# Optimization experiments

Hardware: AMD Instinct MI355X
Metric: run time of the kernel (lower is better)

Reference implementation:

```python
import jax, jax.numpy as jnp
import numpy as np

N_NODES = 50000
N_EDGES = 600000
H_DIM = 128
N_RELS = 8
N_BASES = 4


def setup_inputs() -> dict:
    key = jax.random.key(0)
    ks = jax.random.split(key, 12)
    feats = jax.random.normal(ks[0], (N_NODES, H_DIM), dtype=jnp.float32)
    src = jax.random.randint(ks[1], (N_EDGES,), 0, N_NODES, dtype=jnp.int64)
    dst = jax.random.randint(ks[2], (N_EDGES,), 0, N_NODES, dtype=jnp.int64)
    etype = jax.random.randint(ks[3], (N_EDGES,), 0, N_RELS, dtype=jnp.int64)
    norm = jax.random.uniform(ks[4], (N_EDGES, 1), dtype=jnp.float32)
    s = 1.0 / np.sqrt(H_DIM)
    # layer 0 params (basis decomposition: W_r = sum_b comp[r,b] * basis[b])
    basis0 = jax.random.normal(ks[5], (N_BASES, H_DIM, H_DIM), dtype=jnp.float32) * s
    comp0 = jax.random.normal(ks[6], (N_RELS, N_BASES), dtype=jnp.float32)
    bias0 = jnp.zeros((H_DIM,), dtype=jnp.float32)
    # layer 1 params
    basis1 = jax.random.normal(ks[7], (N_BASES, H_DIM, H_DIM), dtype=jnp.float32) * s
    comp1 = jax.random.normal(ks[8], (N_RELS, N_BASES), dtype=jnp.float32)
    bias1 = jnp.zeros((H_DIM,), dtype=jnp.float32)
    return {"feats": feats, "src": src, "dst": dst, "etype": etype, "norm": norm,
            "basis0": basis0, "comp0": comp0, "bias0": bias0,
            "basis1": basis1, "comp1": comp1, "bias1": bias1}


def _rel_graph_conv(h, src, dst, etype, norm, basis, comp, bias):
    # basis-decomposed relation weights: [R, d_in, d_out]
    W = jnp.einsum('rb,bdo->rdo', comp, basis)
    # transform all nodes under every relation: [R, N, d_out]
    Hr = jnp.einsum('nd,rdo->rno', h, W)
    # gather per-edge message by (relation, source node), apply edge norm
    msg = Hr[etype, src] * norm  # [E, d_out]
    # scatter-sum into destination nodes
    agg = jax.ops.segment_sum(msg, dst, num_segments=h.shape[0])
    return jax.nn.relu(agg + bias)


def reference(feats, src, dst, etype, norm, basis0, comp0, bias0, basis1, comp1, bias1):
    h = _rel_graph_conv(feats, src, dst, etype, norm, basis0, comp0, bias0)
    h = _rel_graph_conv(h, src, dst, etype, norm, basis1, comp1, bias1)
    return h
```

## Files before the change

### kernel.cpp

```cpp
#include <hip/hip_runtime.h>

#define H    128
#define NB   4
#define DT   32

typedef __attribute__((ext_vector_type(8))) short short8;
typedef __attribute__((ext_vector_type(4))) float f32x4;

static __device__ __forceinline__ unsigned short f2bf(float f) {
    unsigned u = __float_as_uint(f);
    unsigned r = (u + 0x7fffu + ((u >> 16) & 1u)) >> 16;
    return (unsigned short)r;
}
static __device__ __forceinline__ float bf_lo(unsigned v) {
    return __uint_as_float((v & 0xffffu) << 16);
}
static __device__ __forceinline__ float bf_hi(unsigned v) {
    return __uint_as_float(v & 0xffff0000u);
}
static __device__ __forceinline__ float bfe(short s) {
    return __uint_as_float(((unsigned)(unsigned short)s) << 16);
}

__global__ __launch_bounds__(256) void zero_i(int* __restrict__ p, int n) {
    int i = blockIdx.x * 256 + threadIdx.x;
    if (i < n) p[i] = 0;
}

__global__ __launch_bounds__(256) void hist_rank(const int* __restrict__ dst,
                                                 int* __restrict__ counts,
                                                 int* __restrict__ rank, int E) {
    int e = blockIdx.x * 256 + threadIdx.x;
    if (e < E) rank[e] = atomicAdd(&counts[dst[e]], 1);
}

__global__ __launch_bounds__(1024) void scan_blocks(const int* __restrict__ counts,
                                                    int* __restrict__ partial,
                                                    int* __restrict__ blocksums, int n) {
    __shared__ int buf[1024];
    int tid = threadIdx.x;
    int i = blockIdx.x * 1024 + tid;
    buf[tid] = (i < n) ? counts[i] : 0;
    __syncthreads();
#pragma unroll
    for (int off = 1; off < 1024; off <<= 1) {
        int t = (tid >= off) ? buf[tid - off] : 0;
        __syncthreads();
        buf[tid] += t;
        __syncthreads();
    }
    if (i < n) partial[i] = buf[tid];
    if (tid == 1023) blocksums[blockIdx.x] = buf[1023];
}

__global__ __launch_bounds__(64) void scan_carry(int* __restrict__ blocksums, int nb) {
    int tid = threadIdx.x;
    int v = (tid < nb) ? blocksums[tid] : 0;
#pragma unroll
    for (int off = 1; off < 64; off <<= 1) {
        int t = __shfl_up(v, off);
        if (tid >= off) v += t;
    }
    if (tid < nb) blocksums[tid] = v;
}

__global__ __launch_bounds__(256) void scan_add(const int* __restrict__ partial,
                                                const int* __restrict__ blocksums,
                                                int* __restrict__ offs, int n) {
    int i = blockIdx.x * 256 + threadIdx.x;
    if (i >= n) return;
    int b = i >> 10;
    int carry = (b > 0) ? blocksums[b - 1] : 0;
    offs[i + 1] = partial[i] + carry;
    if (i == 0) offs[0] = 0;
}

__global__ __launch_bounds__(256) void scatter_edges(
        const int* __restrict__ src, const int* __restrict__ dst,
        const int* __restrict__ etype, const float* __restrict__ norm,
        const float* __restrict__ comp0, const float* __restrict__ comp1,
        const int* __restrict__ offs, const int* __restrict__ rank,
        uint4* __restrict__ er0, uint4* __restrict__ er1, int E) {
    int e = blockIdx.x * 256 + threadIdx.x;
    if (e >= E) return;
    int pos = offs[dst[e]] + rank[e];
    float w = norm[e];
    int et = etype[e];
    float4 c0 = *(const float4*)(comp0 + et * NB);
    float4 c1 = *(const float4*)(comp1 + et * NB);
    uint4 r0, r1;
    r0.x = (unsigned)src[e];
    r0.y = (unsigned)f2bf(w * c0.x) | ((unsigned)f2bf(w * c0.y) << 16);
    r0.z = (unsigned)f2bf(w * c0.z) | ((unsigned)f2bf(w * c0.w) << 16);
    r0.w = 0;
    r1.x = (unsigned)src[e];
    r1.y = (unsigned)f2bf(w * c1.x) | ((unsigned)f2bf(w * c1.y) << 16);
    r1.z = (unsigned)f2bf(w * c1.z) | ((unsigned)f2bf(w * c1.w) << 16);
    r1.w = 0;
    er0[pos] = r0;
    er1[pos] = r1;
}

__global__ __launch_bounds__(256) void convert_bf16(const float* __restrict__ in,
                                                    unsigned short* __restrict__ out, int n4) {
    int i = blockIdx.x * 256 + threadIdx.x;
    if (i >= n4) return;
    float4 v = ((const float4*)in)[i];
    ushort4 o;
    o.x = f2bf(v.x); o.y = f2bf(v.y); o.z = f2bf(v.z); o.w = f2bf(v.w);
    ((ushort4*)out)[i] = o;
}

__global__ __launch_bounds__(128) void make_wb(
        const float* __restrict__ basis0, const float* __restrict__ basis1,
        unsigned short* __restrict__ Wb) {
    int b = blockIdx.x;
    int d = blockIdx.y;
    int l = blockIdx.z;
    int o = threadIdx.x;
    const float* basis = l ? basis1 : basis0;
    float s = basis[((size_t)b * H + d) * H + o];
    Wb[((size_t)l * H + o) * (NB * H) + b * H + d] = f2bf(s);
}

#define EDGE_ACC(REC, HV) {                                             \
    float wa = bf_lo(REC.y), wb = bf_hi(REC.y);                         \
    float wc = bf_lo(REC.z), wd = bf_hi(REC.z);                         \
    _Pragma("unroll")                                                   \
    for (int c = 0; c < 8; ++c) {                                       \
        float f = bfe(HV[c]);                                           \
        a0[c] = fmaf(wa, f, a0[c]); a1[c] = fmaf(wb, f, a1[c]);         \
        a2[c] = fmaf(wc, f, a2[c]); a3[c] = fmaf(wd, f, a3[c]);         \
    } }

__global__ __launch_bounds__(512) void fused_layer(
        const unsigned short* __restrict__ hin,
        const int* __restrict__ offs,
        const uint4* __restrict__ er,
        const unsigned short* __restrict__ Wb,
        const float* __restrict__ bias,
        void* __restrict__ outp, int M, int write_bf16) {
    __shared__ char lds[DT * 1024];
    const int tid  = threadIdx.x;
    const int nl   = tid >> 4;
    const int ch   = tid & 15;
    const int v0   = blockIdx.x * DT;
    const int v    = v0 + nl;

    float a0[8], a1[8], a2[8], a3[8];
#pragma unroll
    for (int c = 0; c < 8; ++c) { a0[c] = 0.f; a1[c] = 0.f; a2[c] = 0.f; a3[c] = 0.f; }

    if (v < M) {
        const int beg = offs[v], end = offs[v + 1];
        int e = beg;
        for (; e + 2 <= end; e += 2) {
            uint4 r0 = er[e];
            uint4 r1 = er[e + 1];
            short8 h0 = *(const short8*)(hin + (size_t)r0.x * H + ch * 8);
            short8 h1 = *(const short8*)(hin + (size_t)r1.x * H + ch * 8);
            EDGE_ACC(r0, h0)
            EDGE_ACC(r1, h1)
        }
        if (e < end) {
            uint4 r0 = er[e];
            short8 h0 = *(const short8*)(hin + (size_t)r0.x * H + ch * 8);
            EDGE_ACC(r0, h0)
        }
    }

    {
        char* row = lds + nl * 1024;
        const int swz = (nl & 7) << 4;
        uint4 pk;
#define PACK(A) pk.x = (unsigned)f2bf(A[0]) | ((unsigned)f2bf(A[1]) << 16); \
                pk.y = (unsigned)f2bf(A[2]) | ((unsigned)f2bf(A[3]) << 16); \
                pk.z = (unsigned)f2bf(A[4]) | ((unsigned)f2bf(A[5]) << 16); \
                pk.w = (unsigned)f2bf(A[6]) | ((unsigned)f2bf(A[7]) << 16);
        PACK(a0) *(uint4*)(row + ((0 * 256 + ch * 16) ^ swz)) = pk;
        PACK(a1) *(uint4*)(row + ((1 * 256 + ch * 16) ^ swz)) = pk;
        PACK(a2) *(uint4*)(row + ((2 * 256 + ch * 16) ^ swz)) = pk;
        PACK(a3) *(uint4*)(row + ((3 * 256 + ch * 16) ^ swz)) = pk;
#undef PACK
    }
    __syncthreads();

    const int wid  = tid >> 6;
    const int lane = tid & 63;
    const int n0 = wid * 16;
    const int lr = lane & 15;
    const int lg = lane >> 4;
    const char* bbase = (const char*)Wb + (size_t)(n0 + lr) * (NB * H) * 2;
    const int swz = (lr & 7) << 4;

    f32x4 acc0 = (f32x4){0.f, 0.f, 0.f, 0.f};
    f32x4 acc1 = (f32x4){0.f, 0.f, 0.f, 0.f};
#pragma unroll
    for (int ks = 0; ks < 16; ++ks) {
        const int kb = ks * 64 + lg * 16;
        short8 b  = *(const short8*)(bbase + kb);
        short8 av0 = *(const short8*)(lds + (lr)      * 1024 + (kb ^ swz));
        short8 av1 = *(const short8*)(lds + (16 + lr) * 1024 + (kb ^ swz));
        acc0 = __builtin_amdgcn_mfma_f32_16x16x32_bf16(av0, b, acc0, 0, 0, 0);
        acc1 = __builtin_amdgcn_mfma_f32_16x16x32_bf16(av1, b, acc1, 0, 0, 0);
    }

    const float bcol = bias[n0 + lr];
#pragma unroll
    for (int m = 0; m < 2; ++m) {
        const f32x4 a = m ? acc1 : acc0;
#pragma unroll
        for (int j = 0; j < 4; ++j) {
            const int rl   = m * 16 + lg * 4 + j;
            const int grow = v0 + rl;
            if (grow < M) {
                float val = fmaxf(a[j] + bcol, 0.f);
                if (write_bf16)
                    ((unsigned short*)outp)[(size_t)grow * H + n0 + lr] = f2bf(val);
                else
                    ((float*)outp)[(size_t)grow * H + n0 + lr] = val;
            }
        }
    }
}

extern "C" void kernel_launch(void* const* d_in, const int* in_sizes, int n_in,
                              void* d_out, int out_size, void* d_ws, size_t ws_size,
                              hipStream_t stream) {
    const float* feats  = (const float*)d_in[0];
    const int*   src    = (const int*)  d_in[1];
    const int*   dst    = (const int*)  d_in[2];
    const int*   etype  = (const int*)  d_in[3];
    const float* norm   = (const float*)d_in[4];
    const float* basis0 = (const float*)d_in[5];
    const float* comp0  = (const float*)d_in[6];
    const float* bias0  = (const float*)d_in[7];
    const float* basis1 = (const float*)d_in[8];
    const float* comp1  = (const float*)d_in[9];
    const float* bias1  = (const float*)d_in[10];
    float* out = (float*)d_out;

    const int M = in_sizes[0] / H;
    const int E = in_sizes[1];

    char* ws = (char*)d_ws;
    size_t cur = 0;
    auto take = [&](size_t bytes) { void* p = ws + cur; cur += (bytes + 255) & ~(size_t)255; return p; };
    unsigned short* hbf  = (unsigned short*)take((size_t)M * H * 2);
    unsigned short* h1bf = (unsigned short*)take((size_t)M * H * 2);
    unsigned short* Wb   = (unsigned short*)take((size_t)2 * H * NB * H * 2);
    int*   counts  = (int*)take((size_t)M * 4);
    int*   offs    = (int*)take((size_t)(M + 1) * 4);
    int*   partial = (int*)take((size_t)M * 4);
    int*   bsums   = (int*)take((size_t)64 * 4);
    int*   rank    = (int*)take((size_t)E * 4);
    uint4* er0     = (uint4*)take((size_t)E * 16);
    uint4* er1     = (uint4*)take((size_t)E * 16);

    dim3 blk(256);
    int mb  = (M + 255) / 256;
    int eb  = (E + 255) / 256;
    int n4  = M * H / 4;
    int cb  = (n4 + 255) / 256;
    int nsb = (M + 1023) / 1024;
    int fb  = (M + DT - 1) / DT;

    zero_i       <<<mb, blk, 0, stream>>>(counts, M);
    hist_rank    <<<eb, blk, 0, stream>>>(dst, counts, rank, E);
    scan_blocks  <<<nsb, 1024, 0, stream>>>(counts, partial, bsums, M);
    scan_carry   <<<1, 64, 0, stream>>>(bsums, nsb);
    scan_add     <<<mb, blk, 0, stream>>>(partial, bsums, offs, M);
    scatter_edges<<<eb, blk, 0, stream>>>(src, dst, etype, norm, comp0, comp1,
                                          offs, rank, er0, er1, E);
    convert_bf16 <<<cb, blk, 0, stream>>>(feats, hbf, n4);
    make_wb      <<<dim3(NB, H, 2), 128, 0, stream>>>(basis0, basis1, Wb);

    fused_layer<<<fb, 512, 0, stream>>>(hbf, offs, er0, Wb, bias0, h1bf, M, 1);
    fused_layer<<<fb, 512, 0, stream>>>(h1bf, offs, er1,
                                        Wb + (size_t)H * NB * H, bias1, out, M, 0);
}
```

Before: 191.6 us.

## Use 32 threads per node with LDS-staged edge records and 16-node blocks

The fused layer now assigns 32 threads per destination node, each handling 4 channels, so a block covers 16 nodes instead of 32. Edge records are loaded cooperatively into LDS in chunks of 32 and then read by all lanes, and the gather loop is unrolled by 4 edges to keep more loads in flight. The GEMM phase now runs a single 16-row MFMA tile per wave, and launch bounds request higher occupancy. This trades more blocks and repeated Wb reads per block for better latency hiding in the irregular gather. Lanes in a node group write and read recs without a barrier between them, so correctness relies on implicit wavefront lockstep.

```diff
diff --git a/kernel.cpp b/kernel.cpp
--- a/kernel.cpp
+++ b/kernel.cpp
@@ -2,7 +2,7 @@
 
 #define H    128
 #define NB   4
-#define DT   32
+#define NPB  16
 
 typedef __attribute__((ext_vector_type(8))) short short8;
 typedef __attribute__((ext_vector_type(4))) float f32x4;
@@ -17,9 +17,6 @@
 }
 static __device__ __forceinline__ float bf_hi(unsigned v) {
     return __uint_as_float(v & 0xffff0000u);
-}
-static __device__ __forceinline__ float bfe(short s) {
-    return __uint_as_float(((unsigned)(unsigned short)s) << 16);
 }
 
 __global__ __launch_bounds__(256) void zero_i(int* __restrict__ p, int n) {
@@ -123,65 +120,73 @@
     Wb[((size_t)l * H + o) * (NB * H) + b * H + d] = f2bf(s);
 }
 
-#define EDGE_ACC(REC, HV) {                                             \
-    float wa = bf_lo(REC.y), wb = bf_hi(REC.y);                         \
-    float wc = bf_lo(REC.z), wd = bf_hi(REC.z);                         \
-    _Pragma("unroll")                                                   \
-    for (int c = 0; c < 8; ++c) {                                       \
-        float f = bfe(HV[c]);                                           \
-        a0[c] = fmaf(wa, f, a0[c]); a1[c] = fmaf(wb, f, a1[c]);         \
-        a2[c] = fmaf(wc, f, a2[c]); a3[c] = fmaf(wd, f, a3[c]);         \
-    } }
-
-__global__ __launch_bounds__(512) void fused_layer(
+#define EACC(R, HV) {                                                   \
+    float f0 = bf_lo(HV.x), f1 = bf_hi(HV.x);                           \
+    float f2 = bf_lo(HV.y), f3 = bf_hi(HV.y);                           \
+    float wa = bf_lo(R.y), wb = bf_hi(R.y);                             \
+    float wc = bf_lo(R.z), wd = bf_hi(R.z);                             \
+    a0[0] = fmaf(wa, f0, a0[0]); a0[1] = fmaf(wa, f1, a0[1]);           \
+    a0[2] = fmaf(wa, f2, a0[2]); a0[3] = fmaf(wa, f3, a0[3]);           \
+    a1[0] = fmaf(wb, f0, a1[0]); a1[1] = fmaf(wb, f1, a1[1]);           \
+    a1[2] = fmaf(wb, f2, a1[2]); a1[3] = fmaf(wb, f3, a1[3]);           \
+    a2[0] = fmaf(wc, f0, a2[0]); a2[1] = fmaf(wc, f1, a2[1]);           \
+    a2[2] = fmaf(wc, f2, a2[2]); a2[3] = fmaf(wc, f3, a2[3]);           \
+    a3[0] = fmaf(wd, f0, a3[0]); a3[1] = fmaf(wd, f1, a3[1]);           \
+    a3[2] = fmaf(wd, f2, a3[2]); a3[3] = fmaf(wd, f3, a3[3]); }
+
+__global__ __launch_bounds__(512, 8) void fused_layer(
         const unsigned short* __restrict__ hin,
         const int* __restrict__ offs,
         const uint4* __restrict__ er,
         const unsigned short* __restrict__ Wb,
         const float* __restrict__ bias,
         void* __restrict__ outp, int M, int write_bf16) {
-    __shared__ char lds[DT * 1024];
-    const int tid  = threadIdx.x;
-    const int nl   = tid >> 4;
-    const int ch   = tid & 15;
-    const int v0   = blockIdx.x * DT;
-    const int v    = v0 + nl;
-
-    float a0[8], a1[8], a2[8], a3[8];
-#pragma unroll
-    for (int c = 0; c < 8; ++c) { a0[c] = 0.f; a1[c] = 0.f; a2[c] = 0.f; a3[c] = 0.f; }
+    __shared__ unsigned short tile[NPB][512];
+    __shared__ uint4 recs[NPB][32];
+    const int tid = threadIdx.x;
+    const int nl  = tid >> 5;
+    const int ch  = tid & 31;
+    const int v0  = blockIdx.x * NPB;
+    const int v   = v0 + nl;
+
+    float a0[4], a1[4], a2[4], a3[4];
+#pragma unroll
+    for (int c = 0; c < 4; ++c) { a0[c] = 0.f; a1[c] = 0.f; a2[c] = 0.f; a3[c] = 0.f; }
 
     if (v < M) {
         const int beg = offs[v], end = offs[v + 1];
-        int e = beg;
-        for (; e + 2 <= end; e += 2) {
-            uint4 r0 = er[e];
-            uint4 r1 = er[e + 1];
-            short8 h0 = *(const short8*)(hin + (size_t)r0.x * H + ch * 8);
-            short8 h1 = *(const short8*)(hin + (size_t)r1.x * H + ch * 8);
-            EDGE_ACC(r0, h0)
-            EDGE_ACC(r1, h1)
+        for (int base = beg; base < end; base += 32) {
+            const int cnt = min(32, end - base);
+            if (ch < cnt) recs[nl][ch] = er[base + ch];
+            int j = 0;
+            for (; j + 4 <= cnt; j += 4) {
+                uint4 r0 = recs[nl][j];
+                uint4 r1 = recs[nl][j + 1];
+                uint4 r2 = recs[nl][j + 2];
+                uint4 r3 = recs[nl][j + 3];
+                uint2 h0 = *(const uint2*)(hin + (size_t)r0.x * H + ch * 4);
+                uint2 h1 = *(const uint2*)(hin + (size_t)r1.x * H + ch * 4);
+                uint2 h2 = *(const uint2*)(hin + (size_t)r2.x * H + ch * 4);
+                uint2 h3 = *(const uint2*)(hin + (size_t)r3.x * H + ch * 4);
+                EACC(r0, h0) EACC(r1, h1) EACC(r2, h2) EACC(r3, h3)
+            }
+            for (; j < cnt; ++j) {
+                uint4 r0 = recs[nl][j];
+                uint2 h0 = *(const uint2*)(hin + (size_t)r0.x * H + ch * 4);
+                EACC(r0, h0)
+            }
         }
-        if (e < end) {
-            uint4 r0 = er[e];
-            short8 h0 = *(const short8*)(hin + (size_t)r0.x * H + ch * 8);
-            EDGE_ACC(r0, h0)
-        }
     }
 
     {
-        char* row = lds + nl * 1024;
+        char* row = (char*)tile[nl];
         const int swz = (nl & 7) << 4;
-        uint4 pk;
-#define PACK(A) pk.x = (unsigned)f2bf(A[0]) | ((unsigned)f2bf(A[1]) << 16); \
-                pk.y = (unsigned)f2bf(A[2]) | ((unsigned)f2bf(A[3]) << 16); \
-                pk.z = (unsigned)f2bf(A[4]) | ((unsigned)f2bf(A[5]) << 16); \
-                pk.w = (unsigned)f2bf(A[6]) | ((unsigned)f2bf(A[7]) << 16);
-        PACK(a0) *(uint4*)(row + ((0 * 256 + ch * 16) ^ swz)) = pk;
-        PACK(a1) *(uint4*)(row + ((1 * 256 + ch * 16) ^ swz)) = pk;
-        PACK(a2) *(uint4*)(row + ((2 * 256 + ch * 16) ^ swz)) = pk;
-        PACK(a3) *(uint4*)(row + ((3 * 256 + ch * 16) ^ swz)) = pk;
-#undef PACK
+#define PUT(B, A) { uint2 pk; \
+        pk.x = (unsigned)f2bf(A[0]) | ((unsigned)f2bf(A[1]) << 16); \
+        pk.y = (unsigned)f2bf(A[2]) | ((unsigned)f2bf(A[3]) << 16); \
+        *(uint2*)(row + ((B * 256 + ch * 8) ^ swz)) = pk; }
+        PUT(0, a0) PUT(1, a1) PUT(2, a2) PUT(3, a3)
+#undef PUT
     }
     __syncthreads();
 
@@ -191,35 +196,28 @@
     const int lr = lane & 15;
     const int lg = lane >> 4;
     const char* bbase = (const char*)Wb + (size_t)(n0 + lr) * (NB * H) * 2;
+    const char* abase = (const char*)tile + lr * 1024;
     const int swz = (lr & 7) << 4;
 
-    f32x4 acc0 = (f32x4){0.f, 0.f, 0.f, 0.f};
-    f32x4 acc1 = (f32x4){0.f, 0.f, 0.f, 0.f};
+    f32x4 acc = (f32x4){0.f, 0.f, 0.f, 0.f};
 #pragma unroll
     for (int ks = 0; ks < 16; ++ks) {
         const int kb = ks * 64 + lg * 16;
-        short8 b  = *(const short8*)(bbase + kb);
-        short8 av0 = *(const short8*)(lds + (lr)      * 1024 + (kb ^ swz));
-        short8 av1 = *(const short8*)(lds + (16 + lr) * 1024 + (kb ^ swz));
-        acc0 = __builtin_amdgcn_mfma_f32_16x16x32_bf16(av0, b, acc0, 0, 0, 0);
-        acc1 = __builtin_amdgcn_mfma_f32_16x16x32_bf16(av1, b, acc1, 0, 0, 0);
+        short8 b = *(const short8*)(bbase + kb);
+        short8 a = *(const short8*)(abase + (kb ^ swz));
+        acc = __builtin_amdgcn_mfma_f32_16x16x32_bf16(a, b, acc, 0, 0, 0);
     }
 
     const float bcol = bias[n0 + lr];
 #pragma unroll
-    for (int m = 0; m < 2; ++m) {
-        const f32x4 a = m ? acc1 : acc0;
-#pragma unroll
-        for (int j = 0; j < 4; ++j) {
-            const int rl   = m * 16 + lg * 4 + j;
-            const int grow = v0 + rl;
-            if (grow < M) {
-                float val = fmaxf(a[j] + bcol, 0.f);
-                if (write_bf16)
-                    ((unsigned short*)outp)[(size_t)grow * H + n0 + lr] = f2bf(val);
-                else
-                    ((float*)outp)[(size_t)grow * H + n0 + lr] = val;
-            }
+    for (int j = 0; j < 4; ++j) {
+        const int grow = v0 + lg * 4 + j;
+        if (grow < M) {
+            float val = fmaxf(acc[j] + bcol, 0.f);
+            if (write_bf16)
+                ((unsigned short*)outp)[(size_t)grow * H + n0 + lr] = f2bf(val);
+            else
+                ((float*)outp)[(size_t)grow * H + n0 + lr] = val;
         }
     }
 }
@@ -263,7 +261,7 @@
     int n4  = M * H / 4;
     int cb  = (n4 + 255) / 256;
     int nsb = (M + 1023) / 1024;
-    int fb  = (M + DT - 1) / DT;
+    int fb  = (M + NPB - 1) / NPB;
 
     zero_i       <<<mb, blk, 0, stream>>>(counts, M);
     hist_rank    <<<eb, blk, 0, stream>>>(dst, counts, rank, E);
```

Measured after the change: 212.6 us. +11.0%, slower.

## Interleave edge records and software-pipeline 4-way edge gather loop

Applied to the files above, without the earlier changes.

Edge records for both layers are interleaved into a single 32-byte-strided array, and the weights move to the z/w fields. The aggregation loop is unrolled four ways and prefetches the next four edge records while the current feature rows are gathered and accumulated. Launch bounds now request 4 blocks per CU. The aim is to hide latency on the dependent load chain from record to feature row. In exchange, each record fetch reads half-used cache lines because of the stride, and the occupancy hint may cause register spills.

```diff
diff --git a/kernel.cpp b/kernel.cpp
--- a/kernel.cpp
+++ b/kernel.cpp
@@ -80,7 +80,7 @@
         const int* __restrict__ etype, const float* __restrict__ norm,
         const float* __restrict__ comp0, const float* __restrict__ comp1,
         const int* __restrict__ offs, const int* __restrict__ rank,
-        uint4* __restrict__ er0, uint4* __restrict__ er1, int E) {
+        uint4* __restrict__ er2, int E) {
     int e = blockIdx.x * 256 + threadIdx.x;
     if (e >= E) return;
     int pos = offs[dst[e]] + rank[e];
@@ -88,17 +88,16 @@
     int et = etype[e];
     float4 c0 = *(const float4*)(comp0 + et * NB);
     float4 c1 = *(const float4*)(comp1 + et * NB);
+    unsigned s = (unsigned)src[e];
     uint4 r0, r1;
-    r0.x = (unsigned)src[e];
-    r0.y = (unsigned)f2bf(w * c0.x) | ((unsigned)f2bf(w * c0.y) << 16);
-    r0.z = (unsigned)f2bf(w * c0.z) | ((unsigned)f2bf(w * c0.w) << 16);
-    r0.w = 0;
-    r1.x = (unsigned)src[e];
-    r1.y = (unsigned)f2bf(w * c1.x) | ((unsigned)f2bf(w * c1.y) << 16);
-    r1.z = (unsigned)f2bf(w * c1.z) | ((unsigned)f2bf(w * c1.w) << 16);
-    r1.w = 0;
-    er0[pos] = r0;
-    er1[pos] = r1;
+    r0.x = s; r0.y = 0;
+    r0.z = (unsigned)f2bf(w * c0.x) | ((unsigned)f2bf(w * c0.y) << 16);
+    r0.w = (unsigned)f2bf(w * c0.z) | ((unsigned)f2bf(w * c0.w) << 16);
+    r1.x = s; r1.y = 0;
+    r1.z = (unsigned)f2bf(w * c1.x) | ((unsigned)f2bf(w * c1.y) << 16);
+    r1.w = (unsigned)f2bf(w * c1.z) | ((unsigned)f2bf(w * c1.w) << 16);
+    er2[(size_t)pos * 2]     = r0;
+    er2[(size_t)pos * 2 + 1] = r1;
 }
 
 __global__ __launch_bounds__(256) void convert_bf16(const float* __restrict__ in,
@@ -123,9 +122,9 @@
     Wb[((size_t)l * H + o) * (NB * H) + b * H + d] = f2bf(s);
 }
 
-#define EDGE_ACC(REC, HV) {                                             \
-    float wa = bf_lo(REC.y), wb = bf_hi(REC.y);                         \
-    float wc = bf_lo(REC.z), wd = bf_hi(REC.z);                         \
+#define EACC(REC, HV) {                                                 \
+    float wa = bf_lo(REC.z), wb = bf_hi(REC.z);                         \
+    float wc = bf_lo(REC.w), wd = bf_hi(REC.w);                         \
     _Pragma("unroll")                                                   \
     for (int c = 0; c < 8; ++c) {                                       \
         float f = bfe(HV[c]);                                           \
@@ -133,7 +132,7 @@
         a2[c] = fmaf(wc, f, a2[c]); a3[c] = fmaf(wd, f, a3[c]);         \
     } }
 
-__global__ __launch_bounds__(512) void fused_layer(
+__global__ __launch_bounds__(512, 4) void fused_layer(
         const unsigned short* __restrict__ hin,
         const int* __restrict__ offs,
         const uint4* __restrict__ er,
@@ -153,19 +152,29 @@
 
     if (v < M) {
         const int beg = offs[v], end = offs[v + 1];
-        int e = beg;
-        for (; e + 2 <= end; e += 2) {
-            uint4 r0 = er[e];
-            uint4 r1 = er[e + 1];
+        const int n = end - beg;
+        const int nfull = n & ~3;
+        const uint4* ep = er + (size_t)beg * 2;
+        uint4 r0, r1, r2, r3;
+        if (nfull > 0) { r0 = ep[0]; r1 = ep[2]; r2 = ep[4]; r3 = ep[6]; }
+        for (int i = 0; i + 4 <= nfull; i += 4) {
             short8 h0 = *(const short8*)(hin + (size_t)r0.x * H + ch * 8);
             short8 h1 = *(const short8*)(hin + (size_t)r1.x * H + ch * 8);
-            EDGE_ACC(r0, h0)
-            EDGE_ACC(r1, h1)
+            short8 h2 = *(const short8*)(hin + (size_t)r2.x * H + ch * 8);
+            short8 h3 = *(const short8*)(hin + (size_t)r3.x * H + ch * 8);
+            uint4 s0, s1, s2, s3;
+            const bool more = (i + 8 <= nfull);
+            if (more) {
+                const uint4* np = ep + (size_t)(i + 4) * 2;
+                s0 = np[0]; s1 = np[2]; s2 = np[4]; s3 = np[6];
+            }
+            EACC(r0, h0) EACC(r1, h1) EACC(r2, h2) EACC(r3, h3)
+            if (more) { r0 = s0; r1 = s1; r2 = s2; r3 = s3; }
         }
-        if (e < end) {
-            uint4 r0 = er[e];
-            short8 h0 = *(const short8*)(hin + (size_t)r0.x * H + ch * 8);
-            EDGE_ACC(r0, h0)
+        for (int e = nfull; e < n; ++e) {
+            uint4 rr = ep[(size_t)e * 2];
+            short8 hh = *(const short8*)(hin + (size_t)rr.x * H + ch * 8);
+            EACC(rr, hh)
         }
     }
 
@@ -198,7 +207,7 @@
 #pragma unroll
     for (int ks = 0; ks < 16; ++ks) {
         const int kb = ks * 64 + lg * 16;
-        short8 b  = *(const short8*)(bbase + kb);
+        short8 b   = *(const short8*)(bbase + kb);
         short8 av0 = *(const short8*)(lds + (lr)      * 1024 + (kb ^ swz));
         short8 av1 = *(const short8*)(lds + (16 + lr) * 1024 + (kb ^ swz));
         acc0 = __builtin_amdgcn_mfma_f32_16x16x32_bf16(av0, b, acc0, 0, 0, 0);
@@ -254,8 +263,7 @@
     int*   partial = (int*)take((size_t)M * 4);
     int*   bsums   = (int*)take((size_t)64 * 4);
     int*   rank    = (int*)take((size_t)E * 4);
-    uint4* er0     = (uint4*)take((size_t)E * 16);
-    uint4* er1     = (uint4*)take((size_t)E * 16);
+    uint4* er2     = (uint4*)take((size_t)E * 32);
 
     dim3 blk(256);
     int mb  = (M + 255) / 256;
@@ -271,11 +279,11 @@
     scan_carry   <<<1, 64, 0, stream>>>(bsums, nsb);
     scan_add     <<<mb, blk, 0, stream>>>(partial, bsums, offs, M);
     scatter_edges<<<eb, blk, 0, stream>>>(src, dst, etype, norm, comp0, comp1,
-                                          offs, rank, er0, er1, E);
+                                          offs, rank, er2, E);
     convert_bf16 <<<cb, blk, 0, stream>>>(feats, hbf, n4);
     make_wb      <<<dim3(NB, H, 2), 128, 0, stream>>>(basis0, basis1, Wb);
 
-    fused_layer<<<fb, 512, 0, stream>>>(hbf, offs, er0, Wb, bias0, h1bf, M, 1);
-    fused_layer<<<fb, 512, 0, stream>>>(h1bf, offs, er1,
+    fused_layer<<<fb, 512, 0, stream>>>(hbf, offs, er2, Wb, bias0, h1bf, M, 1);
+    fused_layer<<<fb, 512, 0, stream>>>(h1bf, offs, er2 + 1,
                                         Wb + (size_t)H * NB * H, bias1, out, M, 0);
 }
```

Measured after the change: 230.2 us. 20.2% more time.

## Split fused aggregate+GEMM layer into separate aggregation and MFMA GEMM kernels

Applied to the files above, without the earlier changes.

The fused per-layer kernel is split in two. An aggregation kernel (256 threads, 16 nodes per block, launch bounds for higher occupancy) writes a bf16 per-node basis-aggregate buffer of size M×4×128 to global memory. A separate MFMA GEMM kernel reads that buffer directly from global memory instead of LDS. The aim is to decouple the latency-bound gather from the GEMM and raise occupancy, at the cost of an extra ~51MB global round trip per layer. The zero kernel is also replaced with hipMemsetAsync.

```diff
diff --git a/kernel.cpp b/kernel.cpp
--- a/kernel.cpp
+++ b/kernel.cpp
@@ -2,7 +2,6 @@
 
 #define H    128
 #define NB   4
-#define DT   32
 
 typedef __attribute__((ext_vector_type(8))) short short8;
 typedef __attribute__((ext_vector_type(4))) float f32x4;
@@ -20,11 +19,6 @@
 }
 static __device__ __forceinline__ float bfe(short s) {
     return __uint_as_float(((unsigned)(unsigned short)s) << 16);
-}
-
-__global__ __launch_bounds__(256) void zero_i(int* __restrict__ p, int n) {
-    int i = blockIdx.x * 256 + threadIdx.x;
-    if (i < n) p[i] = 0;
 }
 
 __global__ __launch_bounds__(256) void hist_rank(const int* __restrict__ dst,
@@ -123,7 +117,7 @@
     Wb[((size_t)l * H + o) * (NB * H) + b * H + d] = f2bf(s);
 }
 
-#define EDGE_ACC(REC, HV) {                                             \
+#define EACC(REC, HV) {                                                 \
     float wa = bf_lo(REC.y), wb = bf_hi(REC.y);                         \
     float wc = bf_lo(REC.z), wd = bf_hi(REC.z);                         \
     _Pragma("unroll")                                                   \
@@ -133,74 +127,78 @@
         a2[c] = fmaf(wc, f, a2[c]); a3[c] = fmaf(wd, f, a3[c]);         \
     } }
 
-__global__ __launch_bounds__(512) void fused_layer(
+__global__ __launch_bounds__(256, 8) void agg_nodes(
         const unsigned short* __restrict__ hin,
         const int* __restrict__ offs,
         const uint4* __restrict__ er,
-        const unsigned short* __restrict__ Wb,
-        const float* __restrict__ bias,
-        void* __restrict__ outp, int M, int write_bf16) {
-    __shared__ char lds[DT * 1024];
-    const int tid  = threadIdx.x;
-    const int nl   = tid >> 4;
-    const int ch   = tid & 15;
-    const int v0   = blockIdx.x * DT;
-    const int v    = v0 + nl;
+        unsigned short* __restrict__ agg,
+        int M) {
+    const int tid = threadIdx.x;
+    const int nl  = tid >> 4;
+    const int ch  = tid & 15;
+    const int v   = blockIdx.x * 16 + nl;
+    if (v >= M) return;
 
     float a0[8], a1[8], a2[8], a3[8];
 #pragma unroll
     for (int c = 0; c < 8; ++c) { a0[c] = 0.f; a1[c] = 0.f; a2[c] = 0.f; a3[c] = 0.f; }
 
-    if (v < M) {
-        const int beg = offs[v], end = offs[v + 1];
-        int e = beg;
-        for (; e + 2 <= end; e += 2) {
-            uint4 r0 = er[e];
-            uint4 r1 = er[e + 1];
-            short8 h0 = *(const short8*)(hin + (size_t)r0.x * H + ch * 8);
-            short8 h1 = *(const short8*)(hin + (size_t)r1.x * H + ch * 8);
-            EDGE_ACC(r0, h0)
-            EDGE_ACC(r1, h1)
-        }
-        if (e < end) {
-            uint4 r0 = er[e];
-            short8 h0 = *(const short8*)(hin + (size_t)r0.x * H + ch * 8);
-            EDGE_ACC(r0, h0)
-        }
-    }
-
-    {
-        char* row = lds + nl * 1024;
-        const int swz = (nl & 7) << 4;
-        uint4 pk;
+    const int beg = offs[v], end = offs[v + 1];
+    int e = beg;
+    for (; e + 2 <= end; e += 2) {
+        uint4 r0 = er[e];
+        uint4 r1 = er[e + 1];
+        short8 h0 = *(const short8*)(hin + (size_t)r0.x * H + ch * 8);
+        short8 h1 = *(const short8*)(hin + (size_t)r1.x * H + ch * 8);
+        EACC(r0, h0)
+        EACC(r1, h1)
+    }
+    if (e < end) {
+        uint4 r0 = er[e];
+        short8 h0 = *(const short8*)(hin + (size_t)r0.x * H + ch * 8);
+        EACC(r0, h0)
+    }
+
+    unsigned short* orow = agg + (size_t)v * (NB * H) + ch * 8;
+    uint4 pk;
 #define PACK(A) pk.x = (unsigned)f2bf(A[0]) | ((unsigned)f2bf(A[1]) << 16); \
                 pk.y = (unsigned)f2bf(A[2]) | ((unsigned)f2bf(A[3]) << 16); \
                 pk.z = (unsigned)f2bf(A[4]) | ((unsigned)f2bf(A[5]) << 16); \
                 pk.w = (unsigned)f2bf(A[6]) | ((unsigned)f2bf(A[7]) << 16);
-        PACK(a0) *(uint4*)(row + ((0 * 256 + ch * 16) ^ swz)) = pk;
-        PACK(a1) *(uint4*)(row + ((1 * 256 + ch * 16) ^ swz)) = pk;
-        PACK(a2) *(uint4*)(row + ((2 * 256 + ch * 16) ^ swz)) = pk;
-        PACK(a3) *(uint4*)(row + ((3 * 256 + ch * 16) ^ swz)) = pk;
+    PACK(a0) *(uint4*)(orow + 0 * H) = pk;
+    PACK(a1) *(uint4*)(orow + 1 * H) = pk;
+    PACK(a2) *(uint4*)(orow + 2 * H) = pk;
+    PACK(a3) *(uint4*)(orow + 3 * H) = pk;
 #undef PACK
-    }
-    __syncthreads();
-
+}
+
+__global__ __launch_bounds__(512) void gemm_out(
+        const unsigned short* __restrict__ agg,
+        const unsigned short* __restrict__ Wb,
+        const float* __restrict__ bias,
+        void* __restrict__ outp, int M, int write_bf16) {
+    const int tid  = threadIdx.x;
     const int wid  = tid >> 6;
     const int lane = tid & 63;
-    const int n0 = wid * 16;
-    const int lr = lane & 15;
-    const int lg = lane >> 4;
-    const char* bbase = (const char*)Wb + (size_t)(n0 + lr) * (NB * H) * 2;
-    const int swz = (lr & 7) << 4;
+    const int v0   = blockIdx.x * 32;
+    const int n0   = wid * 16;
+    const int lr   = lane & 15;
+    const int lg   = lane >> 4;
+
+    const int ar0 = min(v0 + lr, M - 1);
+    const int ar1 = min(v0 + 16 + lr, M - 1);
+    const char* bbase  = (const char*)Wb + (size_t)(n0 + lr) * (NB * H) * 2;
+    const char* a0base = (const char*)(agg + (size_t)ar0 * (NB * H));
+    const char* a1base = (const char*)(agg + (size_t)ar1 * (NB * H));
 
     f32x4 acc0 = (f32x4){0.f, 0.f, 0.f, 0.f};
     f32x4 acc1 = (f32x4){0.f, 0.f, 0.f, 0.f};
 #pragma unroll
     for (int ks = 0; ks < 16; ++ks) {
         const int kb = ks * 64 + lg * 16;
-        short8 b  = *(const short8*)(bbase + kb);
-        short8 av0 = *(const short8*)(lds + (lr)      * 1024 + (kb ^ swz));
-        short8 av1 = *(const short8*)(lds + (16 + lr) * 1024 + (kb ^ swz));
+        short8 b   = *(const short8*)(bbase + kb);
+        short8 av0 = *(const short8*)(a0base + kb);
+        short8 av1 = *(const short8*)(a1base + kb);
         acc0 = __builtin_amdgcn_mfma_f32_16x16x32_bf16(av0, b, acc0, 0, 0, 0);
         acc1 = __builtin_amdgcn_mfma_f32_16x16x32_bf16(av1, b, acc1, 0, 0, 0);
     }
@@ -248,6 +246,7 @@
     auto take = [&](size_t bytes) { void* p = ws + cur; cur += (bytes + 255) & ~(size_t)255; return p; };
     unsigned short* hbf  = (unsigned short*)take((size_t)M * H * 2);
     unsigned short* h1bf = (unsigned short*)take((size_t)M * H * 2);
+    unsigned short* agg  = (unsigned short*)take((size_t)M * NB * H * 2);
     unsigned short* Wb   = (unsigned short*)take((size_t)2 * H * NB * H * 2);
     int*   counts  = (int*)take((size_t)M * 4);
     int*   offs    = (int*)take((size_t)(M + 1) * 4);
@@ -258,14 +257,15 @@
     uint4* er1     = (uint4*)take((size_t)E * 16);
 
     dim3 blk(256);
-    int mb  = (M + 255) / 256;
     int eb  = (E + 255) / 256;
     int n4  = M * H / 4;
     int cb  = (n4 + 255) / 256;
+    int mb  = (M + 255) / 256;
     int nsb = (M + 1023) / 1024;
-    int fb  = (M + DT - 1) / DT;
-
-    zero_i       <<<mb, blk, 0, stream>>>(counts, M);
+    int ab  = (M + 15) / 16;
+    int gb  = (M + 31) / 32;
+
+    hipMemsetAsync(counts, 0, (size_t)M * 4, stream);
     hist_rank    <<<eb, blk, 0, stream>>>(dst, counts, rank, E);
     scan_blocks  <<<nsb, 1024, 0, stream>>>(counts, partial, bsums, M);
     scan_carry   <<<1, 64, 0, stream>>>(bsums, nsb);
@@ -275,7 +275,8 @@
     convert_bf16 <<<cb, blk, 0, stream>>>(feats, hbf, n4);
     make_wb      <<<dim3(NB, H, 2), 128, 0, stream>>>(basis0, basis1, Wb);
 
-    fused_layer<<<fb, 512, 0, stream>>>(hbf, offs, er0, Wb, bias0, h1bf, M, 1);
-    fused_layer<<<fb, 512, 0, stream>>>(h1bf, offs, er1,
-                                        Wb + (size_t)H * NB * H, bias1, out, M, 0);
-}
+    agg_nodes<<<ab, blk, 0, stream>>>(hbf, offs, er0, agg, M);
+    gemm_out <<<gb, 512, 0, stream>>>(agg, Wb, bias0, h1bf, M, 1);
+    agg_nodes<<<ab, blk, 0, stream>>>(h1bf, offs, er1, agg, M);
+    gemm_out <<<gb, 512, 0, stream>>>(agg, Wb + (size_t)H * NB * H, bias1, out, M, 0);
+}
```

New measurement: 295.0 us. 1.54x slower.
